# Optimization experiments

Measured on AMD Instinct MI355X. Metric: run time of the kernel, lower is better.

## Reference

```python
import jax, jax.numpy as jnp
import numpy as np

IGNORE = 255
KA = 10.0
ITERS = 10
BETA = 0.8


def _l2(x, axis):
    # F.normalize(p=2): divide by max(norm, eps)
    return x / jnp.maximum(jnp.linalg.norm(x, axis=axis, keepdims=True), 1e-12)


def setup_inputs() -> dict:
    key = jax.random.key(0)
    k1, k2, k3, k4 = jax.random.split(key, 4)
    B, K, P, C = 8, 19, 16384, 256
    return {
        "logit": jax.random.normal(k1, (B, K, P), jnp.float32),
        "target": jax.random.randint(k2, (B, P), 0, K, jnp.int32),
        "feat": jax.random.normal(k3, (B, C, P), jnp.float32),
        "epoch": 60,
        "prototypes_dataset": _l2(jax.random.normal(k4, (C, K), jnp.float32), 0),
    }


def reference(logit, target, feat, epoch, prototypes_dataset):
    B, K, P = logit.shape
    C = feat.shape[1]
    dt = feat.dtype

    # scatter-sum per-class prototypes over all (b, p) positions; ignore bucket = K
    index = jnp.where(target == IGNORE, K, target).reshape(-1)            # [B*P]
    feat_flat = jnp.swapaxes(feat, 1, 2).reshape(B * P, C)                # [B*P, C]
    proto = jax.ops.segment_sum(feat_flat, index, num_segments=K + 1)    # [K+1, C]
    counts = jax.ops.segment_sum(jnp.ones_like(index), index, num_segments=K + 1)
    prototypes_sum = proto[:K].T                                          # [C, K]
    counts_batch = counts[:K]                                             # [K]

    # epoch is a static python int; epoch >= start_epoch(51) -> full vMF branch
    feat_norm = _l2(feat, 1)                                              # [B, C, P]
    u_init = _l2(prototypes_sum / (counts_batch.astype(dt) + 1e-6), 0)    # [C, K]
    mask0 = counts_batch == 0
    u = _l2(jnp.where(mask0[None, :], prototypes_dataset, u_init), 0)     # 'part' init
    a = jnp.full((1, 1, K), 1.0 / K, dt)

    dis = jnp.einsum('bcp,ck->bpk', feat_norm, u)                         # [B, P, K]
    e = a * jnp.exp(KA * dis)
    p = e / jnp.sum(e, -1, keepdims=True)
    for _ in range(ITERS):
        # 'avmf': second assignment in torch overwrites -> mean over batch, [1, P, K]
        a = jnp.mean(p, 0, keepdims=True)
        # 'uvmf': new prototypes from soft assignments
        u = _l2(jnp.mean(jnp.einsum('bcp,bpk->bck', feat_norm, p), 0), 0)
        dis = jnp.einsum('bcp,ck->bpk', feat_norm, u)
        e = a * jnp.exp(KA * dis)
        p = e / jnp.sum(e, -1, keepdims=True)

    # vMF_hard_loss computed in torch but 'hard' not in loss_type -> not added
    vmf_loss = jnp.mean(-p * (jnp.log(a + 1e-6) + KA * dis)) / float(np.log(K))
    consist_loss = jnp.mean(-jnp.swapaxes(p, 1, 2) * jax.nn.log_softmax(logit, axis=1))

    # contrast: off-diagonal prototype similarity over classes present in batch
    m = (~mask0).astype(dt)
    gram = u_init.T @ u_init                                              # [K, K]
    Kn = jnp.sum(m)
    contrast_loss = (jnp.sum(gram * (m[:, None] * m[None, :])) - Kn) / (Kn * (Kn - 1))

    # 'tce': truncated CE, clamp per-pixel loss at -log(beta)
    logp = jax.nn.log_softmax(logit, axis=1)                              # [B, K, P]
    safe_t = jnp.where(target == IGNORE, 0, target)
    ce = -jnp.take_along_axis(logp, safe_t[:, None, :], axis=1)[:, 0, :]  # [B, P]
    valid = (target != IGNORE).astype(dt)
    loss = jnp.sum(jnp.maximum(ce, -float(np.log(BETA))) * valid) / (jnp.sum(valid) + 1e-6)

    loss = loss + vmf_loss + contrast_loss + consist_loss
    return (loss, jax.lax.stop_gradient(prototypes_sum), jax.lax.stop_gradient(counts_batch))
```

## Files before the change

### kernel.cpp

```cpp
#include <hip/hip_runtime.h>
#include <hip/hip_bf16.h>
#include <math.h>

#define BB 8
#define KK 19
#define PP 16384
#define CC 256
#define NN (BB*PP)
#define KA_C 10.0f
#define IGNORE_L 255
#define CETHR 0.22314355131420976f
#define AQ 524288

#define OFF_FEATN   0
#define OFF_FEATNT  16777216
#define OFF_PROTO   33554432
#define OFF_COUNTS  (OFF_PROTO+4864)
#define OFF_SCAL    (OFF_COUNTS+32)
#define OFF_UINIT   (OFF_SCAL+16)
#define OFF_U       (OFF_UINIT+4864)
#define OFF_UBF     (OFF_U+4864)
#define OFF_A       (OFF_UBF+4224)
#define OFF_UPART   (OFF_A+4*AQ)
#define OFF_R1      (OFF_UPART+2490368)
#define OFF_NORM    (OFF_R1+77824)
#define OFF_LOGT    (OFF_NORM+131072)

typedef __attribute__((ext_vector_type(8))) short short8v;
typedef __attribute__((ext_vector_type(4))) float f32x4;

static __device__ __forceinline__ float bflo(unsigned int v){
    union{unsigned int i; float f;} x; x.i = v << 16; return x.f;
}
static __device__ __forceinline__ unsigned short f2bf(float f){
    union{float f; unsigned int i;} x; x.f = f;
    unsigned int r = (x.i + 0x7fffu + ((x.i >> 16) & 1u)) >> 16;
    return (unsigned short)r;
}
static __device__ __forceinline__ float rowsum16(float v){
    v += __shfl_xor(v,1); v += __shfl_xor(v,2);
    v += __shfl_xor(v,4); v += __shfl_xor(v,8);
    return v;
}
static __device__ __forceinline__ float rowmax16(float v){
    v = fmaxf(v, __shfl_xor(v,1)); v = fmaxf(v, __shfl_xor(v,2));
    v = fmaxf(v, __shfl_xor(v,4)); v = fmaxf(v, __shfl_xor(v,8));
    return v;
}

__global__ __launch_bounds__(256) void counts_kernel(const int* __restrict__ target,
                                                     float* __restrict__ ws) {
    __shared__ int cnt[KK];
    if (threadIdx.x < KK) cnt[threadIdx.x]=0;
    __syncthreads();
    for (int i = blockIdx.x*256 + threadIdx.x; i < NN; i += gridDim.x*256) {
        int t = target[i];
        if (t >= 0 && t < KK) atomicAdd(&cnt[t], 1);
    }
    __syncthreads();
    if (threadIdx.x < KK) atomicAdd(&ws[OFF_COUNTS + threadIdx.x], (float)cnt[threadIdx.x]);
}

__global__ __launch_bounds__(256) void ssct_kernel(const float* __restrict__ feat,
                                                   unsigned short* __restrict__ featn,
                                                   unsigned short* __restrict__ featn_T,
                                                   float* __restrict__ normf) {
    __shared__ float part[4][64];
    __shared__ float rn_lds[64];
    __shared__ unsigned short tTus[64][270];
    int blk = blockIdx.x;
    int b = blk >> 8;
    int px0 = (blk & 255) * 64;
    int tid = threadIdx.x;
    int l = tid & 63, w = tid >> 6;
    const float* fb = feat + (size_t)b*CC*PP;
    int c0 = w*64;
    float fv[64];
    float ss = 0.f;
#pragma unroll
    for (int cc=0; cc<64; cc++) {
        fv[cc] = fb[(size_t)(c0+cc)*PP + px0 + l];
        ss = fmaf(fv[cc], fv[cc], ss);
    }
    part[w][l] = ss;
    __syncthreads();
    if (tid < 64) {
        float s = part[0][tid]+part[1][tid]+part[2][tid]+part[3][tid];
        float nrm = fmaxf(sqrtf(s), 1e-12f);
        normf[(size_t)b*PP + px0 + tid] = nrm;
        rn_lds[tid] = 1.0f/nrm;
    }
    __syncthreads();
    float r = rn_lds[l];
    unsigned short* ob  = featn + (size_t)b*CC*PP + px0;
#pragma unroll
    for (int cc=0; cc<64; cc++) {
        int c = c0 + cc;
        unsigned short us = f2bf(fv[cc] * r);
        ob[(size_t)c*PP + l] = us;
        tTus[l][c] = us;
    }
    __syncthreads();
    unsigned short* obT = featn_T + ((size_t)b*PP + px0)*CC;
    for (int j=0; j<32; j++) {
        int flat = j*256 + tid;
        int px = flat >> 7, cu = flat & 127;
        unsigned int v = *(const unsigned int*)&tTus[px][cu*2];
        *(unsigned int*)&obT[(size_t)px*CC + cu*2] = v;
    }
}

__global__ __launch_bounds__(256) void logt_kernel(const float* __restrict__ logit,
                                                   float* __restrict__ logt) {
    __shared__ float t[256][21];
    int blk = blockIdx.x;
    int b = blk >> 6;
    int px0 = (blk & 63) * 256;
    int tid = threadIdx.x;
    for (int k=0;k<KK;k++)
        t[tid][k] = logit[((size_t)b*KK + k)*PP + px0 + tid];
    __syncthreads();
    float* dst = logt + ((size_t)b*PP + px0)*20;
    for (int j=0; j<20; j++) {
        int flat = j*256 + tid;
        int px = flat / 20, k = flat % 20;
        dst[flat] = (k<KK) ? t[px][k] : 0.f;
    }
}

__global__ __launch_bounds__(256) void proto_mfma_kernel(const unsigned short* __restrict__ featn,
                                                         const int* __restrict__ target,
                                                         const float* __restrict__ normf,
                                                         float* __restrict__ upart) {
    __shared__ int tgt_lds[4][64];
    __shared__ unsigned short nrm_lds[4][64];
    int tid = threadIdx.x;
    int blk = blockIdx.x;
    int pxtile = blk & 255;
    int bgrp = blk >> 8;
    {
        int bi = tid >> 6, j = tid & 63;
        int bb = bgrp*4 + bi;
        tgt_lds[bi][j] = target[(size_t)bb*PP + pxtile*64 + j];
        nrm_lds[bi][j] = f2bf(normf[(size_t)bb*PP + pxtile*64 + j]);
    }
    __syncthreads();
    int lane = tid & 63, wid = tid >> 6;
    int g = lane >> 4, lc = lane & 15;

    f32x4 upacc[4][2];
#pragma unroll
    for (int m=0;m<4;m++)
#pragma unroll
        for (int n=0;n<2;n++) upacc[m][n] = (f32x4){0.f,0.f,0.f,0.f};

    for (int bi=0; bi<4; bi++) {
        int bb = bgrp*4 + bi;
        union { unsigned int u[4]; short8v s; } bfr[2][2];
#pragma unroll
        for (int ks=0; ks<2; ks++) {
            int pxo = ks*32 + g*8;
#pragma unroll
            for (int j2=0;j2<4;j2++) {
                int p0i = pxo + 2*j2, p1i = pxo + 2*j2 + 1;
                int t0 = tgt_lds[bi][p0i], t1 = tgt_lds[bi][p1i];
                unsigned int n0 = nrm_lds[bi][p0i], n1 = nrm_lds[bi][p1i];
                int kk1 = lc + 16;
                bfr[ks][0].u[j2] = (t0==lc ? n0:0u) | ((t1==lc ? n1:0u)<<16);
                bfr[ks][1].u[j2] = (t0==kk1? n0:0u) | ((t1==kk1? n1:0u)<<16);
            }
        }
#pragma unroll
        for (int m=0;m<4;m++) {
            int c = wid*64 + m*16 + lc;
            const unsigned short* fr = featn + ((size_t)bb*CC + c)*PP + pxtile*64;
#pragma unroll
            for (int ks=0; ks<2; ks++) {
                int pxo = ks*32 + g*8;
                union { uint4 u4; short8v s; } af2;
                af2.u4 = *(const uint4*)&fr[pxo];
                upacc[m][0] = __builtin_amdgcn_mfma_f32_16x16x32_bf16(af2.s, bfr[ks][0].s, upacc[m][0], 0,0,0);
                upacc[m][1] = __builtin_amdgcn_mfma_f32_16x16x32_bf16(af2.s, bfr[ks][1].s, upacc[m][1], 0,0,0);
            }
        }
    }
#pragma unroll
    for (int m=0;m<4;m++) {
        int cb = wid*64 + m*16 + g*4;
#pragma unroll
        for (int n=0;n<2;n++) {
            int kk = lc + 16*n;
            if (kk < KK) {
#pragma unroll
                for (int r=0;r<4;r++)
                    upart[(size_t)blk*4864 + (size_t)(cb+r)*KK + kk] = upacc[m][n][r];
            }
        }
    }
}

__global__ __launch_bounds__(256) void setup_kernel(const float* __restrict__ pd,
                                                    float* __restrict__ ws) {
    int c = threadIdx.x;
    __shared__ float red[256];
    __shared__ float nrm[KK];
    __shared__ float lds_ui[256][KK];
    float cnts[KK], vi[KK];
#pragma unroll
    for (int k=0;k<KK;k++) cnts[k] = ws[OFF_COUNTS+k];
#pragma unroll
    for (int k=0;k<KK;k++) vi[k] = ws[OFF_PROTO + c*KK + k] / (cnts[k] + 1e-6f);
    for (int k=0;k<KK;k++) {
        red[c] = vi[k]*vi[k];
        __syncthreads();
        for (int s=128;s>0;s>>=1){ if (c<s) red[c]+=red[c+s]; __syncthreads(); }
        if (c==0) nrm[k] = fmaxf(sqrtf(red[0]), 1e-12f);
        __syncthreads();
    }
#pragma unroll
    for (int k=0;k<KK;k++) { vi[k] = vi[k]/nrm[k]; lds_ui[c][k] = vi[k]; ws[OFF_UINIT + c*KK + k] = vi[k]; }
    __syncthreads();
    float w0[KK];
#pragma unroll
    for (int k=0;k<KK;k++) w0[k] = (cnts[k]==0.f) ? pd[c*KK+k] : vi[k];
    for (int k=0;k<KK;k++) {
        red[c] = w0[k]*w0[k];
        __syncthreads();
        for (int s=128;s>0;s>>=1){ if (c<s) red[c]+=red[c+s]; __syncthreads(); }
        if (c==0) nrm[k] = fmaxf(sqrtf(red[0]), 1e-12f);
        __syncthreads();
    }
    unsigned short* ubf = (unsigned short*)(ws + OFF_UBF);
#pragma unroll
    for (int k=0;k<KK;k++) {
        float uv = w0[k] / nrm[k];
        ws[OFF_U + k*CC + c] = uv;
        ubf[k*264 + c] = f2bf(uv);
    }
    float m[KK]; float Kn=0.f;
#pragma unroll
    for (int k=0;k<KK;k++){ m[k] = (cnts[k]==0.f)?0.f:1.f; Kn += m[k]; }
    float csum = 0.f;
    for (int idx = c; idx < KK*KK; idx += 256) {
        int k1 = idx / KK, k2 = idx % KK;
        if (m[k1]!=0.f && m[k2]!=0.f) {
            float gg=0.f;
            for (int cc2=0; cc2<CC; cc2++) gg += lds_ui[cc2][k1]*lds_ui[cc2][k2];
            csum += gg;
        }
    }
    red[c]=csum; __syncthreads();
    for (int s=128;s>0;s>>=1){ if (c<s) red[c]+=red[c+s]; __syncthreads(); }
    if (c==0) ws[OFF_SCAL+4] = (red[0] - Kn) / (Kn * (Kn - 1.f));
}

__global__ __launch_bounds__(256) void pu_kernel(const unsigned short* __restrict__ featn,
                                                 const unsigned short* __restrict__ featn_T,
                                                 const unsigned short* __restrict__ ubf,
                                                 const float* __restrict__ aRbase,
                                                 float* __restrict__ aWbase,
                                                 float* __restrict__ upart,
                                                 int uniform_a) {
    __shared__ __attribute__((aligned(16))) unsigned short u_lds[32*264];
    __shared__ __attribute__((aligned(16))) unsigned short p_lds[32*72];
    int tid = threadIdx.x;
    {
        const uint4* src = (const uint4*)ubf;
        uint4* dst = (uint4*)u_lds;
        for (int i=tid; i<1056; i+=256) dst[i] = src[i];
    }
    __syncthreads();
    int blk = blockIdx.x;
    int pxtile = blk & 255;
    int bgrp = blk >> 8;
    int lane = tid & 63, wid = tid >> 6;
    int g = lane >> 4, lc = lane & 15;
    int px_w = pxtile*64 + wid*16;

    float a0r[4], a1r[4];
    if (uniform_a) {
#pragma unroll
        for (int r=0;r<4;r++){ a0r[r]=1.0f/(float)KK; a1r[r]=1.0f/(float)KK; }
    } else {
        int k1 = (lc+16 > KK-1) ? (KK-1) : (lc+16);
#pragma unroll
        for (int r=0;r<4;r++) {
            int pxg = px_w + g*4 + r;
            float s0 = aRbase[0*AQ + (size_t)pxg*32 + lc] + aRbase[1*AQ + (size_t)pxg*32 + lc];
            float s1 = aRbase[0*AQ + (size_t)pxg*32 + k1] + aRbase[1*AQ + (size_t)pxg*32 + k1];
            a0r[r] = s0*0.125f;
            a1r[r] = s1*0.125f;
        }
    }

    f32x4 upacc[4][2];
#pragma unroll
    for (int m=0;m<4;m++)
#pragma unroll
        for (int n=0;n<2;n++) upacc[m][n] = (f32x4){0.f,0.f,0.f,0.f};
    float aacc[2][4];
#pragma unroll
    for (int n=0;n<2;n++)
#pragma unroll
        for (int r=0;r<4;r++) aacc[n][r]=0.f;

    for (int bi=0; bi<4; bi++) {
        int bb = bgrp*4 + bi;
        const unsigned short* fb = featn + (size_t)bb*CC*PP;
        const unsigned short* fTrow = featn_T + ((size_t)bb*PP + px_w + lc)*CC;
        f32x4 acc0 = (f32x4){0.f,0.f,0.f,0.f};
        f32x4 acc1 = (f32x4){0.f,0.f,0.f,0.f};
#pragma unroll
        for (int ks=0; ks<8; ks++) {
            int cbase = ks*32 + g*8;
            union { uint4 u4; short8v s; } af, bf0, bf1;
            af.u4  = *(const uint4*)&fTrow[cbase];
            bf0.u4 = *(const uint4*)&u_lds[(size_t)lc*264 + cbase];
            bf1.u4 = *(const uint4*)&u_lds[(size_t)(lc+16)*264 + cbase];
            acc0 = __builtin_amdgcn_mfma_f32_16x16x32_bf16(af.s, bf0.s, acc0, 0,0,0);
            acc1 = __builtin_amdgcn_mfma_f32_16x16x32_bf16(af.s, bf1.s, acc1, 0,0,0);
        }
#pragma unroll
        for (int r=0;r<4;r++) {
            float e0 = a0r[r] * __expf(KA_C * acc0[r]);
            float e1 = (lc+16 < KK) ? a1r[r] * __expf(KA_C * acc1[r]) : 0.f;
            float sv = rowsum16(e0 + e1);
            float inv = 1.0f/sv;
            float p0 = e0*inv, p1 = e1*inv;
            aacc[0][r] += p0; aacc[1][r] += p1;
            int pl = wid*16 + g*4 + r;
            p_lds[(size_t)lc*72 + pl]      = f2bf(p0);
            p_lds[(size_t)(lc+16)*72 + pl] = f2bf(p1);
        }
        __syncthreads();
#pragma unroll
        for (int m=0;m<4;m++) {
            int c = wid*64 + m*16 + lc;
            const unsigned short* fr = fb + (size_t)c*PP + pxtile*64;
#pragma unroll
            for (int ks=0; ks<2; ks++) {
                int pxo = ks*32 + g*8;
                union { uint4 u4; short8v s; } af2, bp0, bp1;
                af2.u4 = *(const uint4*)&fr[pxo];
                bp0.u4 = *(const uint4*)&p_lds[(size_t)lc*72 + pxo];
                bp1.u4 = *(const uint4*)&p_lds[(size_t)(lc+16)*72 + pxo];
                upacc[m][0] = __builtin_amdgcn_mfma_f32_16x16x32_bf16(af2.s, bp0.s, upacc[m][0], 0,0,0);
                upacc[m][1] = __builtin_amdgcn_mfma_f32_16x16x32_bf16(af2.s, bp1.s, upacc[m][1], 0,0,0);
            }
        }
        __syncthreads();
    }
#pragma unroll
    for (int m=0;m<4;m++) {
        int cb = wid*64 + m*16 + g*4;
#pragma unroll
        for (int n=0;n<2;n++) {
            int kk = lc + 16*n;
            if (kk < KK) {
#pragma unroll
                for (int r=0;r<4;r++)
                    upart[(size_t)blk*4864 + (size_t)(cb+r)*KK + kk] = upacc[m][n][r];
            }
        }
    }
    float* aOut = aWbase + (size_t)bgrp*AQ;
#pragma unroll
    for (int n=0;n<2;n++) {
        int kk = lc + 16*n;
        if (kk < KK) {
#pragma unroll
            for (int r=0;r<4;r++) {
                int pxg = px_w + g*4 + r;
                aOut[(size_t)pxg*32 + kk] = aacc[n][r];
            }
        }
    }
}

__global__ __launch_bounds__(256) void r1_kernel(const float* __restrict__ upart,
                                                 float* __restrict__ r1buf) {
    int blk = blockIdx.x;
    int echunk = blk % 19;
    int ichunk = blk / 19;
    int e = echunk*256 + threadIdx.x;
    float s = 0.f;
    int i0 = ichunk*64;
    for (int i=i0; i<i0+64; i++) s += upart[(size_t)i*4864 + e];
    r1buf[(size_t)ichunk*4864 + e] = s;
}

__global__ __launch_bounds__(256) void r2_kernel(const float* __restrict__ r1buf,
                                                 float* __restrict__ ws) {
    int k = blockIdx.x;
    int c = threadIdx.x;
    float s = 0.f;
#pragma unroll
    for (int i=0;i<8;i++) s += r1buf[(size_t)i*4864 + c*KK + k];
    __shared__ float red[256];
    red[c] = s*s; __syncthreads();
    for (int q=128;q>0;q>>=1){ if (c<q) red[c]+=red[c+q]; __syncthreads(); }
    float nrm = fmaxf(sqrtf(red[0]), 1e-12f);
    float uv = s / nrm;
    ws[OFF_U + k*CC + c] = uv;
    ((unsigned short*)(ws + OFF_UBF))[k*264 + c] = f2bf(uv);
}

__global__ __launch_bounds__(256) void protored2_kernel(const float* __restrict__ r1buf,
                                                        float* __restrict__ ws) {
    int e = blockIdx.x*256 + threadIdx.x;
    float s = 0.f;
#pragma unroll
    for (int i=0;i<8;i++) s += r1buf[(size_t)i*4864 + e];
    ws[OFF_PROTO + e] = s;
}

__global__ __launch_bounds__(256) void final_mfma_kernel(const unsigned short* __restrict__ featn_T,
                                                         const float* __restrict__ logt,
                                                         const int* __restrict__ target,
                                                         const unsigned short* __restrict__ ubf,
                                                         const float* __restrict__ aFbase,
                                                         float* __restrict__ scal) {
    __shared__ __attribute__((aligned(16))) unsigned short u_lds[32*264];
    int tid = threadIdx.x;
    {
        const uint4* src = (const uint4*)ubf;
        uint4* dst = (uint4*)u_lds;
        for (int i=tid; i<1056; i+=256) dst[i] = src[i];
    }
    __syncthreads();
    int blk = blockIdx.x;
    int pxtile = blk & 255;
    int bgrp = blk >> 8;
    int lane = tid & 63, wid = tid >> 6;
    int g = lane >> 4, lc = lane & 15;
    int px_w = pxtile*64 + wid*16;
    bool valid1 = (lc+16) < KK;

    float v_vmf=0.f, v_cons=0.f, v_ce=0.f, v_cnt=0.f;

    for (int bi=0; bi<4; bi++) {
        int bb = bgrp*4 + bi;
        const unsigned short* fTrow = featn_T + ((size_t)bb*PP + px_w + lc)*CC;
        f32x4 acc0 = (f32x4){0.f,0.f,0.f,0.f};
        f32x4 acc1 = (f32x4){0.f,0.f,0.f,0.f};
#pragma unroll
        for (int ks=0; ks<8; ks++) {
            int cbase = ks*32 + g*8;
            union { uint4 u4; short8v s; } af, bf0, bf1;
            af.u4  = *(const uint4*)&fTrow[cbase];
            bf0.u4 = *(const uint4*)&u_lds[(size_t)lc*264 + cbase];
            bf1.u4 = *(const uint4*)&u_lds[(size_t)(lc+16)*264 + cbase];
            acc0 = __builtin_amdgcn_mfma_f32_16x16x32_bf16(af.s, bf0.s, acc0, 0,0,0);
            acc1 = __builtin_amdgcn_mfma_f32_16x16x32_bf16(af.s, bf1.s, acc1, 0,0,0);
        }
#pragma unroll
        for (int r=0;r<4;r++) {
            int pxg = px_w + g*4 + r;
            float d0 = acc0[r], d1 = acc1[r];
            float av0 = (aFbase[0*AQ + (size_t)pxg*32 + lc] + aFbase[1*AQ + (size_t)pxg*32 + lc])*0.125f;
            float av1 = 0.f;
            if (valid1) {
                int k1 = lc+16;
                av1 = (aFbase[0*AQ + (size_t)pxg*32 + k1] + aFbase[1*AQ + (size_t)pxg*32 + k1])*0.125f;
            }
            float e0 = av0 * __expf(KA_C * d0);
            float e1 = valid1 ? av1 * __expf(KA_C * d1) : 0.f;
            float den = rowsum16(e0 + e1);
            float inv = 1.0f/den;
            float p0 = e0*inv, p1 = e1*inv;
            float vt = -p0*(__logf(av0+1e-6f) + KA_C*d0);
            if (valid1) vt += -p1*(__logf(av1+1e-6f) + KA_C*d1);
            float vt_row = rowsum16(vt);
            const float* lrow = logt + ((size_t)bb*PP + pxg)*20;
            float lg0 = lrow[lc];
            float lg1 = valid1 ? lrow[lc+16] : -3.4e38f;
            float mx = rowmax16(fmaxf(lg0, lg1));
            float sme = __expf(lg0-mx) + (valid1 ? __expf(lg1-mx) : 0.f);
            sme = rowsum16(sme);
            float lse = mx + __logf(sme);
            float ct = -p0*(lg0-lse);
            if (valid1) ct += -p1*(lg1-lse);
            float ct_row = rowsum16(ct);
            int t = target[(size_t)bb*PP + pxg];
            float ltt = (lc==t ? lg0 : 0.f) + ((valid1 && lc+16==t) ? lg1 : 0.f);
            float lt = rowsum16(ltt);
            if (lc==0) {
                v_vmf += vt_row;
                v_cons += ct_row;
                if (t != IGNORE_L) { v_ce += fmaxf(lse - lt, CETHR); v_cnt += 1.f; }
            }
        }
    }
    __shared__ float red[4][4];
    int w = tid >> 6;
    float v0=v_vmf, v1=v_cons, v2=v_ce, v3=v_cnt;
#pragma unroll
    for (int s=32;s>0;s>>=1) {
        v0 += __shfl_xor(v0, s); v1 += __shfl_xor(v1, s);
        v2 += __shfl_xor(v2, s); v3 += __shfl_xor(v3, s);
    }
    if ((tid&63)==0){ red[w][0]=v0; red[w][1]=v1; red[w][2]=v2; red[w][3]=v3; }
    __syncthreads();
    if (tid==0) {
        atomicAdd(&scal[0], red[0][0]+red[1][0]+red[2][0]+red[3][0]);
        atomicAdd(&scal[1], red[0][1]+red[1][1]+red[2][1]+red[3][1]);
        atomicAdd(&scal[2], red[0][2]+red[1][2]+red[2][2]+red[3][2]);
        atomicAdd(&scal[3], red[0][3]+red[1][3]+red[2][3]+red[3][3]);
    }
}

__global__ __launch_bounds__(256) void finalize_kernel(const float* __restrict__ ws,
                                                       float* __restrict__ out) {
    if (blockIdx.x==0 && threadIdx.x==0) {
        float cnt_all = (float)BB*(float)PP*(float)KK;
        float vmf  = ws[OFF_SCAL+0] / cnt_all / logf((float)KK);
        float cons = ws[OFF_SCAL+1] / cnt_all;
        float ce   = ws[OFF_SCAL+2] / (ws[OFF_SCAL+3] + 1e-6f);
        float contrast = ws[OFF_SCAL+4];
        out[0] = ce + vmf + contrast + cons;
    }
    int i = blockIdx.x*256 + threadIdx.x;
    if (i < 4864) out[1+i] = ws[OFF_PROTO+i];
    if (blockIdx.x==0 && threadIdx.x < KK) out[1+4864+threadIdx.x] = ws[OFF_COUNTS+threadIdx.x];
}

extern "C" void kernel_launch(void* const* d_in, const int* in_sizes, int n_in,
                              void* d_out, int out_size, void* d_ws, size_t ws_size,
                              hipStream_t stream) {
    (void)in_sizes; (void)n_in; (void)out_size; (void)ws_size;
    const float* logit  = (const float*)d_in[0];
    const int*   target = (const int*)d_in[1];
    const float* feat   = (const float*)d_in[2];
    const float* pd     = (const float*)d_in[4];
    float* out = (float*)d_out;
    float* ws  = (float*)d_ws;

    unsigned short* featn   = (unsigned short*)ws;
    unsigned short* featn_T = (unsigned short*)(ws + OFF_FEATNT);
    unsigned short* ubf     = (unsigned short*)(ws + OFF_UBF);
    float* upart = ws + OFF_UPART;
    float* r1buf = ws + OFF_R1;
    float* normf = ws + OFF_NORM;
    float* logt  = ws + OFF_LOGT;
    float* scal  = ws + OFF_SCAL;
    float* aSet[2] = { ws + OFF_A, ws + OFF_A + (size_t)2*AQ };

    hipMemsetAsync(ws + OFF_PROTO, 0, 4912*sizeof(float), stream);
    hipMemsetAsync(ws + OFF_UBF, 0, 4224*sizeof(float), stream);
    ssct_kernel<<<2048, 256, 0, stream>>>(feat, featn, featn_T, normf);
    counts_kernel<<<256, 256, 0, stream>>>(target, ws);
    logt_kernel<<<512, 256, 0, stream>>>(logit, logt);
    proto_mfma_kernel<<<512, 256, 0, stream>>>(featn, target, normf, upart);
    r1_kernel<<<152, 256, 0, stream>>>(upart, r1buf);
    protored2_kernel<<<19, 256, 0, stream>>>(r1buf, ws);
    setup_kernel<<<1, 256, 0, stream>>>(pd, ws);

    for (int t=0; t<10; t++) {
        if (t > 0) {
            r1_kernel<<<152, 256, 0, stream>>>(upart, r1buf);
            r2_kernel<<<KK, 256, 0, stream>>>(r1buf, ws);
        }
        pu_kernel<<<512, 256, 0, stream>>>(featn, featn_T, ubf,
                                           aSet[t&1], aSet[(t+1)&1],
                                           upart, (t==0)?1:0);
    }
    r1_kernel<<<152, 256, 0, stream>>>(upart, r1buf);
    r2_kernel<<<KK, 256, 0, stream>>>(r1buf, ws);
    final_mfma_kernel<<<512, 256, 0, stream>>>(featn_T, logt, target, ubf, aSet[0], scal);
    finalize_kernel<<<20, 256, 0, stream>>>(ws, out);
}
```

Measured before the change: 556.4 us.

## Transpose partial-prototype layout and fuse two-stage reductions into single kernels

Partial prototype sums are now stored block-index-innermost, so a single kernel per class can sum all 512 partials with contiguous float4 loads and then normalize. This replaces the r1/r2 and r1/protored2 kernel pairs and removes about ten launches plus the intermediate buffer. Only 19 blocks now do the full reduction, which limits parallelism, and the producer writes become strided across blocks. The transpose kernel also halves its LDS staging buffer by transposing in two halves, which adds an extra sync round in exchange for possibly better occupancy.

```diff
diff --git a/kernel.cpp b/kernel.cpp
--- a/kernel.cpp
+++ b/kernel.cpp
@@ -22,8 +22,7 @@
 #define OFF_UBF     (OFF_U+4864)
 #define OFF_A       (OFF_UBF+4224)
 #define OFF_UPART   (OFF_A+4*AQ)
-#define OFF_R1      (OFF_UPART+2490368)
-#define OFF_NORM    (OFF_R1+77824)
+#define OFF_NORM    (OFF_UPART+2490368)
 #define OFF_LOGT    (OFF_NORM+131072)
 
 typedef __attribute__((ext_vector_type(8))) short short8v;
@@ -67,7 +66,7 @@
                                                    float* __restrict__ normf) {
     __shared__ float part[4][64];
     __shared__ float rn_lds[64];
-    __shared__ unsigned short tTus[64][270];
+    __shared__ unsigned short tTus[64][136];
     int blk = blockIdx.x;
     int b = blk >> 8;
     int px0 = (blk & 255) * 64;
@@ -96,17 +95,25 @@
 #pragma unroll
     for (int cc=0; cc<64; cc++) {
         int c = c0 + cc;
-        unsigned short us = f2bf(fv[cc] * r);
-        ob[(size_t)c*PP + l] = us;
-        tTus[l][c] = us;
-    }
-    __syncthreads();
+        ob[(size_t)c*PP + l] = f2bf(fv[cc] * r);
+    }
     unsigned short* obT = featn_T + ((size_t)b*PP + px0)*CC;
-    for (int j=0; j<32; j++) {
-        int flat = j*256 + tid;
-        int px = flat >> 7, cu = flat & 127;
-        unsigned int v = *(const unsigned int*)&tTus[px][cu*2];
-        *(unsigned int*)&obT[(size_t)px*CC + cu*2] = v;
+    for (int half=0; half<2; half++) {
+        if ((w>>1) == half) {
+            int cl0 = c0 - half*128;
+#pragma unroll
+            for (int cc=0; cc<64; cc++)
+                tTus[l][cl0+cc] = f2bf(fv[cc] * r);
+        }
+        __syncthreads();
+#pragma unroll
+        for (int j=0; j<16; j++) {
+            int flat = j*256 + tid;
+            int px = flat >> 6, cu = flat & 63;
+            unsigned int v = *(const unsigned int*)&tTus[px][cu*2];
+            *(unsigned int*)&obT[(size_t)px*CC + half*128 + cu*2] = v;
+        }
+        __syncthreads();
     }
 }
 
@@ -193,10 +200,32 @@
             if (kk < KK) {
 #pragma unroll
                 for (int r=0;r<4;r++)
-                    upart[(size_t)blk*4864 + (size_t)(cb+r)*KK + kk] = upacc[m][n][r];
-            }
-        }
-    }
+                    upart[((size_t)(cb+r)*KK + kk)*512 + blk] = upacc[m][n][r];
+            }
+        }
+    }
+}
+
+__global__ __launch_bounds__(256) void protoall_kernel(const float* __restrict__ upart,
+                                                       float* __restrict__ ws) {
+    int k = blockIdx.x;
+    int tid = threadIdx.x;
+    int g16 = tid >> 4, j = tid & 15;
+    __shared__ float su[256];
+    for (int round=0; round<16; round++) {
+        int c = round*16 + g16;
+        const float* row = upart + (size_t)(c*KK + k)*512;
+        float s = 0.f;
+#pragma unroll
+        for (int q=0;q<8;q++) {
+            float4 v = *(const float4*)&row[q*64 + j*4];
+            s += (v.x+v.y)+(v.z+v.w);
+        }
+        s = rowsum16(s);
+        if (j==0) su[c] = s;
+    }
+    __syncthreads();
+    ws[OFF_PROTO + tid*KK + k] = su[tid];
 }
 
 __global__ __launch_bounds__(256) void setup_kernel(const float* __restrict__ pd,
@@ -359,7 +388,7 @@
             if (kk < KK) {
 #pragma unroll
                 for (int r=0;r<4;r++)
-                    upart[(size_t)blk*4864 + (size_t)(cb+r)*KK + kk] = upacc[m][n][r];
+                    upart[((size_t)(cb+r)*KK + kk)*512 + blk] = upacc[m][n][r];
             }
         }
     }
@@ -377,41 +406,34 @@
     }
 }
 
-__global__ __launch_bounds__(256) void r1_kernel(const float* __restrict__ upart,
-                                                 float* __restrict__ r1buf) {
-    int blk = blockIdx.x;
-    int echunk = blk % 19;
-    int ichunk = blk / 19;
-    int e = echunk*256 + threadIdx.x;
-    float s = 0.f;
-    int i0 = ichunk*64;
-    for (int i=i0; i<i0+64; i++) s += upart[(size_t)i*4864 + e];
-    r1buf[(size_t)ichunk*4864 + e] = s;
-}
-
-__global__ __launch_bounds__(256) void r2_kernel(const float* __restrict__ r1buf,
-                                                 float* __restrict__ ws) {
+__global__ __launch_bounds__(256) void rall_kernel(const float* __restrict__ upart,
+                                                   float* __restrict__ ws) {
     int k = blockIdx.x;
-    int c = threadIdx.x;
-    float s = 0.f;
-#pragma unroll
-    for (int i=0;i<8;i++) s += r1buf[(size_t)i*4864 + c*KK + k];
+    int tid = threadIdx.x;
+    int g16 = tid >> 4, j = tid & 15;
+    __shared__ float su[256];
     __shared__ float red[256];
-    red[c] = s*s; __syncthreads();
+    for (int round=0; round<16; round++) {
+        int c = round*16 + g16;
+        const float* row = upart + (size_t)(c*KK + k)*512;
+        float s = 0.f;
+#pragma unroll
+        for (int q=0;q<8;q++) {
+            float4 v = *(const float4*)&row[q*64 + j*4];
+            s += (v.x+v.y)+(v.z+v.w);
+        }
+        s = rowsum16(s);
+        if (j==0) su[c] = s;
+    }
+    __syncthreads();
+    int c = tid;
+    float v = su[c];
+    red[c] = v*v; __syncthreads();
     for (int q=128;q>0;q>>=1){ if (c<q) red[c]+=red[c+q]; __syncthreads(); }
     float nrm = fmaxf(sqrtf(red[0]), 1e-12f);
-    float uv = s / nrm;
+    float uv = v / nrm;
     ws[OFF_U + k*CC + c] = uv;
     ((unsigned short*)(ws + OFF_UBF))[k*264 + c] = f2bf(uv);
-}
-
-__global__ __launch_bounds__(256) void protored2_kernel(const float* __restrict__ r1buf,
-                                                        float* __restrict__ ws) {
-    int e = blockIdx.x*256 + threadIdx.x;
-    float s = 0.f;
-#pragma unroll
-    for (int i=0;i<8;i++) s += r1buf[(size_t)i*4864 + e];
-    ws[OFF_PROTO + e] = s;
 }
 
 __global__ __launch_bounds__(256) void final_mfma_kernel(const unsigned short* __restrict__ featn_T,
@@ -539,7 +561,6 @@
     unsigned short* featn_T = (unsigned short*)(ws + OFF_FEATNT);
     unsigned short* ubf     = (unsigned short*)(ws + OFF_UBF);
     float* upart = ws + OFF_UPART;
-    float* r1buf = ws + OFF_R1;
     float* normf = ws + OFF_NORM;
     float* logt  = ws + OFF_LOGT;
     float* scal  = ws + OFF_SCAL;
@@ -551,21 +572,17 @@
     counts_kernel<<<256, 256, 0, stream>>>(target, ws);
     logt_kernel<<<512, 256, 0, stream>>>(logit, logt);
     proto_mfma_kernel<<<512, 256, 0, stream>>>(featn, target, normf, upart);
-    r1_kernel<<<152, 256, 0, stream>>>(upart, r1buf);
-    protored2_kernel<<<19, 256, 0, stream>>>(r1buf, ws);
+    protoall_kernel<<<KK, 256, 0, stream>>>(upart, ws);
     setup_kernel<<<1, 256, 0, stream>>>(pd, ws);
 
     for (int t=0; t<10; t++) {
-        if (t > 0) {
-            r1_kernel<<<152, 256, 0, stream>>>(upart, r1buf);
-            r2_kernel<<<KK, 256, 0, stream>>>(r1buf, ws);
-        }
+        if (t > 0)
+            rall_kernel<<<KK, 256, 0, stream>>>(upart, ws);
         pu_kernel<<<512, 256, 0, stream>>>(featn, featn_T, ubf,
                                            aSet[t&1], aSet[(t+1)&1],
                                            upart, (t==0)?1:0);
     }
-    r1_kernel<<<152, 256, 0, stream>>>(upart, r1buf);
-    r2_kernel<<<KK, 256, 0, stream>>>(r1buf, ws);
+    rall_kernel<<<KK, 256, 0, stream>>>(upart, ws);
     final_mfma_kernel<<<512, 256, 0, stream>>>(featn_T, logt, target, ubf, aSet[0], scal);
     finalize_kernel<<<20, 256, 0, stream>>>(ws, out);
 }
```

Result: slower. 766.6 us (+37.8%).
